# Optimization experiments

Hardware: AMD Instinct MI355X
Metric: run time of the kernel (lower is better)

## Reference

```python
import jax, jax.numpy as jnp
import numpy as np

T, B, L, D = 4, 16, 1024, 256
TAU = 2.0        # LIF membrane time constant
V_TH = 1.0       # spike threshold
ALPHA = 4.0      # sigmoid surrogate slope (spikingjelly default)


@jax.custom_vjp
def spike(x):
    # Heaviside step with sigmoid surrogate gradient
    return (x >= 0.0).astype(x.dtype)

def _spike_fwd(x):
    return spike(x), x

def _spike_bwd(x, g):
    s = jax.nn.sigmoid(ALPHA * x)
    return (g * ALPHA * s * (1.0 - s),)

spike.defvjp(_spike_fwd, _spike_bwd)


def lif_multistep(x):
    """MultiStepLIFNode(tau=2, hard reset to 0, detach_reset=True) over dim 0.
    x: [T, B, 1, D] -> spikes [T, B, 1, D]."""
    def step(v, xt):
        h = v + (xt - v) / TAU                 # neuronal charge
        s = spike(h - V_TH)                    # fire
        v_next = h * (1.0 - jax.lax.stop_gradient(s))  # detached hard reset
        return v_next, s
    _, spikes = jax.lax.scan(step, jnp.zeros_like(x[0]), x)
    return spikes


def setup_inputs() -> dict:
    key = jax.random.key(0)
    kq, kk, kv, km = jax.random.split(key, 4)
    q = jax.random.normal(kq, (T, B, L, D), jnp.float32)
    k = jax.random.normal(kk, (T, B, L, D), jnp.float32)
    v = jax.random.normal(kv, (T, B, L, D), jnp.float32)
    mask = jax.random.randint(km, (T, B, L), 0, 2) > 0  # bool padding mask
    return {"q": q, "k": k, "v": v, "mask": mask}


def reference(q, k, v, mask):
    # mode='s' path of ScaledDotProductAttention
    attn = k * v                                      # [T,B,L,D]
    attn = jnp.where(mask[..., None], 0.0, attn)      # masked_fill(mask, 0)
    kv = jnp.sum(attn, axis=-2, keepdims=True)        # [T,B,1,D]
    kv = lif_multistep(kv)                            # spiking gate over T
    output = q * kv                                   # broadcast over L
    return output, attn
```

## Files before the change

### kernel.cpp

```cpp
#include <hip/hip_runtime.h>

#define T_ 4
#define B_ 16
#define L_ 1024
#define D_ 256
#define TAU_INV 0.5f
#define V_TH 1.0f

constexpr int TB_   = T_ * B_;
constexpr int NELEM = T_ * B_ * L_ * D_;
constexpr int BD_   = B_ * D_;
constexpr int TBD_  = T_ * B_ * D_;

typedef float f4 __attribute__((ext_vector_type(4)));

#define NCHUNK 32
#define LC 32

__global__ __launch_bounds__(256) void attn_partial_kernel(
    const float* __restrict__ k, const float* __restrict__ v,
    const int* __restrict__ mask, float* __restrict__ attn_out,
    float* __restrict__ partials)
{
    const int tid   = threadIdx.x;
    const int tb    = blockIdx.x / NCHUNK;
    const int chunk = blockIdx.x % NCHUNK;
    const int d4    = (tid & 63) * 4;
    const int rg    = tid >> 6;

    const int base = tb * (L_ * D_);
    f4 acc = (f4)(0.0f);

    #pragma unroll
    for (int i = 0; i < LC / 4; ++i) {
        const int l   = chunk * LC + i * 4 + rg;
        const int off = base + l * D_ + d4;
        const f4 kk = __builtin_nontemporal_load(reinterpret_cast<const f4*>(k + off));
        const f4 vv = __builtin_nontemporal_load(reinterpret_cast<const f4*>(v + off));
        const int m = mask[tb * L_ + l];
        f4 a = m ? (f4)(0.0f) : (kk * vv);
        __builtin_nontemporal_store(a, reinterpret_cast<f4*>(attn_out + off));
        acc += a;
    }

    __shared__ f4 red[256];
    red[tid] = acc;
    __syncthreads();
    if (rg == 0) {
        f4 s = red[tid] + red[tid + 64] + red[tid + 128] + red[tid + 192];
        *reinterpret_cast<f4*>(partials + (tb * NCHUNK + chunk) * D_ + d4) = s;
    }
}

__global__ void lif_kernel(const float* __restrict__ partials,
                           float* __restrict__ spikes)
{
    const int idx = blockIdx.x * blockDim.x + threadIdx.x;
    if (idx >= BD_) return;
    const int b = idx >> 8;
    const int d = idx & 255;

    float vm = 0.0f;
    #pragma unroll
    for (int t = 0; t < T_; ++t) {
        const int tb = t * B_ + b;
        float x = 0.0f;
        #pragma unroll
        for (int c = 0; c < NCHUNK; ++c) {
            x += partials[(tb * NCHUNK + c) * D_ + d];
        }
        const float h = vm + (x - vm) * TAU_INV;
        const float s = (h >= V_TH) ? 1.0f : 0.0f;
        spikes[t * BD_ + idx] = s;
        vm = h * (1.0f - s);
    }
}

__global__ __launch_bounds__(256) void qmul_kernel(
    const float* __restrict__ q, const float* __restrict__ spikes,
    float* __restrict__ out)
{
    const int i4 = blockIdx.x * blockDim.x + threadIdx.x;
    if (i4 >= NELEM / 4) return;
    const int d4  = (i4 & 63) * 4;
    const int tbl = i4 >> 6;
    const int tb  = tbl >> 10;
    const f4 qq = __builtin_nontemporal_load(reinterpret_cast<const f4*>(q) + i4);
    const f4 ss = *reinterpret_cast<const f4*>(spikes + tb * D_ + d4);
    const f4 o  = qq * ss;
    __builtin_nontemporal_store(o, reinterpret_cast<f4*>(out) + i4);
}

extern "C" void kernel_launch(void* const* d_in, const int* in_sizes, int n_in,
                              void* d_out, int out_size, void* d_ws, size_t ws_size,
                              hipStream_t stream) {
    const float* q    = (const float*)d_in[0];
    const float* k    = (const float*)d_in[1];
    const float* v    = (const float*)d_in[2];
    const int*   mask = (const int*)d_in[3];

    float* out  = (float*)d_out;
    float* attn = out + NELEM;

    float* partials = (float*)d_ws;
    float* spikes   = partials + TB_ * NCHUNK * D_;

    attn_partial_kernel<<<TB_ * NCHUNK, 256, 0, stream>>>(k, v, mask, attn, partials);
    lif_kernel<<<(BD_ + 255) / 256, 256, 0, stream>>>(partials, spikes);
    qmul_kernel<<<NELEM / 4 / 256, 256, 0, stream>>>(q, spikes, out);
}
```

Baseline: 263.9 us.

## Fuse LIF into q-multiply kernel and skip k/v loads for masked rows

Removes the separate LIF kernel. Each block of the q-multiply kernel now redundantly reduces the chunk partials for all timesteps of its batch row and runs the LIF recurrence itself before scaling its slice of q. This saves a launch and the spikes round trip through memory, at the cost of repeated partial reads (about 128KB per tb, done by 16 blocks each). The attention kernel also skips the k and v loads for masked rows, which cuts read traffic roughly in half for a random mask but adds divergence.

New measurement: 258.5 us. 1.02x faster.

```diff
diff --git a/kernel.cpp b/kernel.cpp
--- a/kernel.cpp
+++ b/kernel.cpp
@@ -9,8 +9,6 @@
 
 constexpr int TB_   = T_ * B_;
 constexpr int NELEM = T_ * B_ * L_ * D_;
-constexpr int BD_   = B_ * D_;
-constexpr int TBD_  = T_ * B_ * D_;
 
 typedef float f4 __attribute__((ext_vector_type(4)));
 
@@ -23,9 +21,10 @@
     float* __restrict__ partials)
 {
     const int tid   = threadIdx.x;
-    const int tb    = blockIdx.x / NCHUNK;
-    const int chunk = blockIdx.x % NCHUNK;
-    const int d4    = (tid & 63) * 4;
+    const int tb    = blockIdx.x >> 5;
+    const int chunk = blockIdx.x & 31;
+    const int lane  = tid & 63;
+    const int d4    = lane * 4;
     const int rg    = tid >> 6;
 
     const int base = tb * (L_ * D_);
@@ -35,12 +34,17 @@
     for (int i = 0; i < LC / 4; ++i) {
         const int l   = chunk * LC + i * 4 + rg;
         const int off = base + l * D_ + d4;
-        const f4 kk = __builtin_nontemporal_load(reinterpret_cast<const f4*>(k + off));
-        const f4 vv = __builtin_nontemporal_load(reinterpret_cast<const f4*>(v + off));
-        const int m = mask[tb * L_ + l];
-        f4 a = m ? (f4)(0.0f) : (kk * vv);
+        const int m   = mask[tb * L_ + l];
+        f4 a;
+        if (m) {
+            a = (f4)(0.0f);
+        } else {
+            const f4 kk = __builtin_nontemporal_load(reinterpret_cast<const f4*>(k + off));
+            const f4 vv = __builtin_nontemporal_load(reinterpret_cast<const f4*>(v + off));
+            a = kk * vv;
+            acc += a;
+        }
         __builtin_nontemporal_store(a, reinterpret_cast<f4*>(attn_out + off));
-        acc += a;
     }
 
     __shared__ f4 red[256];
@@ -52,43 +56,62 @@
     }
 }
 
-__global__ void lif_kernel(const float* __restrict__ partials,
-                           float* __restrict__ spikes)
-{
-    const int idx = blockIdx.x * blockDim.x + threadIdx.x;
-    if (idx >= BD_) return;
-    const int b = idx >> 8;
-    const int d = idx & 255;
-
-    float vm = 0.0f;
-    #pragma unroll
-    for (int t = 0; t < T_; ++t) {
-        const int tb = t * B_ + b;
-        float x = 0.0f;
-        #pragma unroll
-        for (int c = 0; c < NCHUNK; ++c) {
-            x += partials[(tb * NCHUNK + c) * D_ + d];
-        }
-        const float h = vm + (x - vm) * TAU_INV;
-        const float s = (h >= V_TH) ? 1.0f : 0.0f;
-        spikes[t * BD_ + idx] = s;
-        vm = h * (1.0f - s);
-    }
-}
-
-__global__ __launch_bounds__(256) void qmul_kernel(
-    const float* __restrict__ q, const float* __restrict__ spikes,
+__global__ __launch_bounds__(256) void lif_qmul_kernel(
+    const float* __restrict__ q, const float* __restrict__ partials,
     float* __restrict__ out)
 {
-    const int i4 = blockIdx.x * blockDim.x + threadIdx.x;
-    if (i4 >= NELEM / 4) return;
-    const int d4  = (i4 & 63) * 4;
-    const int tbl = i4 >> 6;
-    const int tb  = tbl >> 10;
-    const f4 qq = __builtin_nontemporal_load(reinterpret_cast<const f4*>(q) + i4);
-    const f4 ss = *reinterpret_cast<const f4*>(spikes + tb * D_ + d4);
-    const f4 o  = qq * ss;
-    __builtin_nontemporal_store(o, reinterpret_cast<f4*>(out) + i4);
+    const int tid  = threadIdx.x;
+    const int tb   = blockIdx.x >> 4;
+    const int c16  = blockIdx.x & 15;
+    const int t    = tb >> 4;
+    const int b    = tb & 15;
+    const int lane = tid & 63;
+    const int d4   = lane * 4;
+    const int rg   = tid >> 6;
+
+    f4 s[T_];
+    #pragma unroll
+    for (int tt = 0; tt < T_; ++tt) {
+        f4 a = (f4)(0.0f);
+        #pragma unroll
+        for (int j = 0; j < 8; ++j) {
+            const int cc = rg * 8 + j;
+            a += *reinterpret_cast<const f4*>(partials + ((tt * B_ + b) * NCHUNK + cc) * D_ + d4);
+        }
+        s[tt] = a;
+    }
+
+    __shared__ f4 red[4][T_][64];
+    #pragma unroll
+    for (int tt = 0; tt < T_; ++tt) red[rg][tt][lane] = s[tt];
+    __syncthreads();
+
+    f4 spike = (f4)(0.0f);
+    {
+        f4 vm = (f4)(0.0f);
+        #pragma unroll
+        for (int tt = 0; tt < T_; ++tt) {
+            const f4 x = red[0][tt][lane] + red[1][tt][lane]
+                       + red[2][tt][lane] + red[3][tt][lane];
+            const f4 h = vm + (x - vm) * TAU_INV;
+            f4 sp;
+            sp.x = (h.x >= V_TH) ? 1.0f : 0.0f;
+            sp.y = (h.y >= V_TH) ? 1.0f : 0.0f;
+            sp.z = (h.z >= V_TH) ? 1.0f : 0.0f;
+            sp.w = (h.w >= V_TH) ? 1.0f : 0.0f;
+            if (tt == t) spike = sp;
+            vm = h * ((f4)(1.0f) - sp);
+        }
+    }
+
+    const int base = tb * (L_ * D_);
+    #pragma unroll
+    for (int i = 0; i < 16; ++i) {
+        const int l   = c16 * 64 + i * 4 + rg;
+        const int off = base + l * D_ + d4;
+        const f4 qq = __builtin_nontemporal_load(reinterpret_cast<const f4*>(q + off));
+        __builtin_nontemporal_store(qq * spike, reinterpret_cast<f4*>(out + off));
+    }
 }
 
 extern "C" void kernel_launch(void* const* d_in, const int* in_sizes, int n_in,
@@ -103,9 +126,7 @@
     float* attn = out + NELEM;
 
     float* partials = (float*)d_ws;
-    float* spikes   = partials + TB_ * NCHUNK * D_;
 
     attn_partial_kernel<<<TB_ * NCHUNK, 256, 0, stream>>>(k, v, mask, attn, partials);
-    lif_kernel<<<(BD_ + 255) / 256, 256, 0, stream>>>(partials, spikes);
-    qmul_kernel<<<NELEM / 4 / 256, 256, 0, stream>>>(q, spikes, out);
+    lif_qmul_kernel<<<TB_ * 16, 256, 0, stream>>>(q, partials, out);
 }
```
